# Kernel tuning notes

Hardware: AMD Instinct MI355X
Metric: run time of the kernel (lower is better)

Reference implementation:

```python
import jax, jax.numpy as jnp
import numpy as np

DIM_MODEL = 1024
DIM_K = 64
DIM_V = 64
H = 16
B = 2
S = 2048


def setup_inputs() -> dict:
    key = jax.random.key(0)
    ks = jax.random.split(key, 11)
    s = 0.02
    return {
        "Q": jax.random.normal(ks[0], (B, S, DIM_MODEL), jnp.float32),
        "K": jax.random.normal(ks[1], (B, S, DIM_MODEL), jnp.float32),
        "V": jax.random.normal(ks[2], (B, S, DIM_MODEL), jnp.float32),
        "Wq": jax.random.normal(ks[3], (DIM_MODEL, H * DIM_K), jnp.float32) * s,
        "bq": jnp.zeros((H * DIM_K,), jnp.float32),
        "Wk": jax.random.normal(ks[4], (DIM_MODEL, H * DIM_K), jnp.float32) * s,
        "bk": jnp.zeros((H * DIM_K,), jnp.float32),
        "Wv": jax.random.normal(ks[5], (DIM_MODEL, H * DIM_V), jnp.float32) * s,
        "bv": jnp.zeros((H * DIM_V,), jnp.float32),
        "Wo": jax.random.normal(ks[6], (H * DIM_V, DIM_MODEL), jnp.float32) * s,
        "bo": jnp.zeros((DIM_MODEL,), jnp.float32),
    }


def reference(Q, K, V, Wq, bq, Wk, bk, Wv, bv, Wo, bo):
    b, len_q = Q.shape[0], Q.shape[1]
    # QKV projections, split heads: [b, h, S, d]
    q = (Q @ Wq + bq).reshape(b, len_q, H, DIM_K).transpose(0, 2, 1, 3)
    k = (K @ Wk + bk).reshape(b, K.shape[1], H, DIM_K).transpose(0, 2, 1, 3)
    v = (V @ Wv + bv).reshape(b, V.shape[1], H, DIM_V).transpose(0, 2, 1, 3)
    # FAITHFUL QUIRK: original scales by sqrt(K.shape[0]) == batch size, not dim_k
    scale = 1.0 / np.sqrt(b).astype(np.float32)
    att = jnp.einsum('bhqd,bhkd->bhqk', q * scale, k)
    att = jax.nn.softmax(att, axis=-1)
    out = jnp.einsum('bhqk,bhkd->bhqd', att, v)  # [b,h,S,dv]
    out = out.transpose(0, 2, 1, 3).reshape(b, len_q, H * DIM_V)
    return out @ Wo + bo
```

## Files before the change

kernel.cpp:

```cpp
#include <hip/hip_runtime.h>
#include <hip/hip_bf16.h>


using bf16 = __hip_bfloat16;
typedef __attribute__((ext_vector_type(4))) float f32x4;
typedef __attribute__((ext_vector_type(8))) short bf16x8;

__device__ __forceinline__ void gload_lds16(const void* gsrc, void* ldst) {
    __builtin_amdgcn_global_load_lds(
        (const __attribute__((address_space(1))) void*)gsrc,
        (__attribute__((address_space(3))) void*)ldst,
        16, 0, 0);
}

__device__ __forceinline__ float fexp2(float x) {
    float r; asm("v_exp_f32 %0, %1" : "=v"(r) : "v"(x)); return r;
}

__device__ __forceinline__ unsigned cvtpk(float a, float b) {
    unsigned d; asm("v_cvt_pk_bf16_f32 %0, %1, %2" : "=v"(d) : "v"(a), "v"(b));
    return d;
}

__device__ __forceinline__ void pls32(unsigned &a, unsigned &b) {
    asm("v_permlane32_swap_b32 %0, %1" : "+v"(a), "+v"(b));
}
__device__ __forceinline__ void pls16(unsigned &a, unsigned &b) {
    asm("v_permlane16_swap_b32 %0, %1" : "+v"(a), "+v"(b));
}

__device__ __forceinline__ unsigned pack2bf(float a, float b) {
    unsigned short ua = __builtin_bit_cast(unsigned short, __float2bfloat16(a));
    unsigned short ub = __builtin_bit_cast(unsigned short, __float2bfloat16(b));
    return (unsigned)ua | ((unsigned)ub << 16);
}

__global__ void conv3_kernel(const float* __restrict__ X0, const float* __restrict__ X1,
                             const float* __restrict__ X2,
                             bf16* __restrict__ O0, bf16* __restrict__ O1, bf16* __restrict__ O2,
                             int n4) {
    int z = blockIdx.z;
    const float* in = z == 0 ? X0 : (z == 1 ? X1 : X2);
    bf16* out = z == 0 ? O0 : (z == 1 ? O1 : O2);
    int idx = blockIdx.x * blockDim.x + threadIdx.x;
    int stride = gridDim.x * blockDim.x;
    for (int i = idx; i < n4; i += stride) {
        float4 v = reinterpret_cast<const float4*>(in)[i];
        reinterpret_cast<uint2*>(out)[i] = make_uint2(pack2bf(v.x, v.y), pack2bf(v.z, v.w));
    }
}

__global__ void transpose4_kernel(const float* __restrict__ W0, const float* __restrict__ W1,
                                  const float* __restrict__ W2, const float* __restrict__ W3,
                                  bf16* __restrict__ T0, bf16* __restrict__ T1,
                                  bf16* __restrict__ T2, bf16* __restrict__ T3) {
    int z = blockIdx.z;
    const float* W = z == 0 ? W0 : (z == 1 ? W1 : (z == 2 ? W2 : W3));
    bf16* WT = z == 0 ? T0 : (z == 1 ? T1 : (z == 2 ? T2 : T3));
    __shared__ float t[32][33];
    int bx = blockIdx.x * 32, by = blockIdx.y * 32;
    int x = threadIdx.x, y = threadIdx.y;
    #pragma unroll
    for (int i = 0; i < 4; ++i)
        t[y + 8*i][x] = W[(size_t)(by + y + 8*i) * 1024 + bx + x];
    __syncthreads();
    #pragma unroll
    for (int i = 0; i < 4; ++i)
        WT[(size_t)(bx + y + 8*i) * 1024 + by + x] = __float2bfloat16(t[x][y + 8*i]);
}

template<int NTILE>
__global__ __launch_bounds__(256, 3)
void gemm_bt(const bf16* __restrict__ A0, const bf16* __restrict__ A1, const bf16* __restrict__ A2,
             const bf16* __restrict__ B0, const bf16* __restrict__ B1, const bf16* __restrict__ B2,
             const float* __restrict__ bi0, const float* __restrict__ bi1, const float* __restrict__ bi2,
             void* __restrict__ O0, void* __restrict__ O1, void* __restrict__ O2,
             int mode_base)
{
    const int f = blockIdx.x;
    int x, y, z;
    if (NTILE == 128) {
        const int s = f >> 3;
        y = s & 7;
        const int t = (f & 7) + 8 * (s >> 3);
        x = t & 31; z = t >> 5;
    } else {
        const int s = f >> 3;
        y = s & 15;
        x = (f & 7) + 8 * (s >> 4);
        z = 0;
    }
    const bf16* A  = z == 0 ? A0 : (z == 1 ? A1 : A2);
    const bf16* BT = z == 0 ? B0 : (z == 1 ? B1 : B2);
    const float* bias = z == 0 ? bi0 : (z == 1 ? bi1 : bi2);
    void* Cout = z == 0 ? O0 : (z == 1 ? O1 : O2);
    const int mode = mode_base + z;

    constexpr int MF = (NTILE == 128) ? 4 : 2;
    __shared__ __align__(16) char Abuf[16384];
    __shared__ __align__(16) char Bbuf[NTILE * 128];
    const int tid = threadIdx.x;
    const int wave = tid >> 6, lane = tid & 63;
    const int g = lane >> 4, ln = lane & 15;
    const int m0 = x * 128, n0 = y * NTILE;
    const int wm = (NTILE == 128) ? (wave >> 1) * 64 : wave * 32;
    const int wn = (NTILE == 128) ? (wave & 1) * 64 : 0;
    const int lnsw = (ln & 7) << 4;

    f32x4 acc[MF][4] = {};

    for (int k0 = 0; k0 < 1024; k0 += 64) {
        __syncthreads();
        #pragma unroll
        for (int rd = 0; rd < 4; ++rd) {
            int row = rd * 32 + (tid >> 3);
            int src = ((tid & 7) * 16) ^ (((tid >> 3) & 7) << 4);
            gload_lds16((const char*)(A + (size_t)(m0 + row) * 1024 + k0) + src,
                        Abuf + rd * 4096 + tid * 16);
        }
        #pragma unroll
        for (int rd = 0; rd < NTILE / 32; ++rd) {
            int row = rd * 32 + (tid >> 3);
            int src = ((tid & 7) * 16) ^ (((tid >> 3) & 7) << 4);
            gload_lds16((const char*)(BT + (size_t)(n0 + row) * 1024 + k0) + src,
                        Bbuf + rd * 4096 + tid * 16);
        }
        __syncthreads();
        #pragma unroll
        for (int kk = 0; kk < 2; ++kk) {
            bf16x8 af[MF], bfr[4];
            #pragma unroll
            for (int mf = 0; mf < MF; ++mf)
                af[mf] = *(const bf16x8*)&Abuf[(wm + mf*16 + ln) * 128 + ((kk*64 + g*16) ^ lnsw)];
            #pragma unroll
            for (int nf = 0; nf < 4; ++nf)
                bfr[nf] = *(const bf16x8*)&Bbuf[(wn + nf*16 + ln) * 128 + ((kk*64 + g*16) ^ lnsw)];
            #pragma unroll
            for (int mf = 0; mf < MF; ++mf)
                #pragma unroll
                for (int nf = 0; nf < 4; ++nf)
                    acc[mf][nf] = __builtin_amdgcn_mfma_f32_16x16x32_bf16(af[mf], bfr[nf], acc[mf][nf], 0, 0, 0);
        }
    }

    const float scl = (mode == 0) ? (0.70710678118654752f * 1.44269504088896340f) : 1.0f;
    #pragma unroll
    for (int mf = 0; mf < MF; ++mf) {
        #pragma unroll
        for (int nf = 0; nf < 4; ++nf) {
            int col = n0 + wn + nf*16 + ln;
            float bv = bias[col];
            #pragma unroll
            for (int r = 0; r < 4; ++r) {
                int row = m0 + wm + mf*16 + g*4 + r;
                float v = (acc[mf][nf][r] + bv) * scl;
                if (mode == 0 || mode == 1) {
                    ((bf16*)Cout)[(size_t)row * 1024 + col] = __float2bfloat16(v);
                } else if (mode == 2) {
                    int b = row >> 11, ss = row & 2047;
                    int hh = col >> 6, dv = col & 63;
                    ((bf16*)Cout)[(((size_t)(b*16 + hh) * 64 + dv) << 11) + ss] = __float2bfloat16(v);
                } else {
                    ((float*)Cout)[(size_t)row * 1024 + col] = v;
                }
            }
        }
    }
}

__global__ __launch_bounds__(256, 2)
void attn_kernel(const bf16* __restrict__ qh, const bf16* __restrict__ kh,
                 const bf16* __restrict__ vt, bf16* __restrict__ aout)
{
    __shared__ __align__(16) bf16 Kls[2][128 * 64];
    __shared__ __align__(16) bf16 Vls[2][64 * 128];
    const int f = blockIdx.x;
    const int xcd = f & 7, s = f >> 3, i = s & 15, ghi = s >> 4;
    const int bh = xcd + 8 * ghi;
    const int b = bh >> 4, h = bh & 15;
    const int q0 = i * 128;

    const int tid = threadIdx.x;
    const int wave = tid >> 6, lane = tid & 63;
    const int g = lane >> 4, ln = lane & 15;
    const int srow = lane >> 3;
    const int scol = ((lane & 7) * 16) ^ ((srow & 7) << 4);
    const int lnsw = (ln & 7) << 4;

    const bf16* kbase = kh + (size_t)(b * 2048) * 1024 + h * 64;
    const bf16* vbase = vt + (size_t)bh * 64 * 2048;

    const int vrow_in = lane >> 4;
    const int vcol16 = lane & 15;

    bf16x8 qf[2][2];
    #pragma unroll
    for (int nf = 0; nf < 2; ++nf) {
        const bf16* qrow = qh + (size_t)(b*2048 + q0 + wave*32 + nf*16 + ln) * 1024 + h*64;
        qf[nf][0] = *(const bf16x8*)(qrow + g*8);
        qf[nf][1] = *(const bf16x8*)(qrow + 32 + g*8);
    }

    auto stageKV = [&](int kv0, int buf) {
        #pragma unroll
        for (int c2 = 0; c2 < 4; ++c2) {
            int c = wave * 4 + c2;
            int krow = c * 8 + srow;
            gload_lds16((const char*)(kbase + (size_t)(kv0 + krow) * 1024) + scol,
                        (char*)&Kls[buf][0] + c * 1024);
        }
        #pragma unroll
        for (int c2 = 0; c2 < 4; ++c2) {
            int c = wave * 4 + c2;
            int vrow = c * 4 + vrow_in;
            int sc16 = vcol16 ^ (vrow & 15);
            gload_lds16((const char*)(vbase + (size_t)vrow * 2048 + kv0) + sc16 * 16,
                        (char*)&Vls[buf][0] + c * 1024);
        }
    };

    stageKV(0, 0);

    f32x4 oacc[4][2] = {};
    f32x4 lacc[2] = {};
    union PU { unsigned u[4]; bf16x8 v; };
    PU ones;
    ones.u[0] = ones.u[1] = ones.u[2] = ones.u[3] = 0x3F803F80u;

    for (int t = 0; t < 16; ++t) {
        const int cur = t & 1;
        if (t < 15) {
            stageKV((t + 1) * 128, cur ^ 1);
            asm volatile("s_waitcnt vmcnt(8)\n\ts_barrier" ::: "memory");
        } else {
            asm volatile("s_waitcnt vmcnt(0)\n\ts_barrier" ::: "memory");
        }
        __builtin_amdgcn_sched_barrier(0);

        const char* Kc = (const char*)&Kls[cur][0];
        const char* Vc = (const char*)&Vls[cur][0];

        f32x4 sacA[4][2] = {}, sacB[4][2] = {};
        __builtin_amdgcn_s_setprio(1);
        #pragma unroll
        for (int kk = 0; kk < 2; ++kk) {
            bf16x8 kf[4];
            #pragma unroll
            for (int mf = 0; mf < 4; ++mf)
                kf[mf] = *(const bf16x8*)(Kc + (mf*16 + ln) * 128 + ((kk*64 + g*16) ^ lnsw));
            #pragma unroll
            for (int mf = 0; mf < 4; ++mf)
                #pragma unroll
                for (int nf = 0; nf < 2; ++nf)
                    sacA[mf][nf] = __builtin_amdgcn_mfma_f32_16x16x32_bf16(kf[mf], qf[nf][kk], sacA[mf][nf], 0, 0, 0);
        }
        #pragma unroll
        for (int kk = 0; kk < 2; ++kk) {
            bf16x8 kf[4];
            #pragma unroll
            for (int mf = 0; mf < 4; ++mf)
                kf[mf] = *(const bf16x8*)(Kc + (64 + mf*16 + ln) * 128 + ((kk*64 + g*16) ^ lnsw));
            #pragma unroll
            for (int mf = 0; mf < 4; ++mf)
                #pragma unroll
                for (int nf = 0; nf < 2; ++nf)
                    sacB[mf][nf] = __builtin_amdgcn_mfma_f32_16x16x32_bf16(kf[mf], qf[nf][kk], sacB[mf][nf], 0, 0, 0);
        }
        __builtin_amdgcn_s_setprio(0);

        #pragma unroll
        for (int ha = 0; ha < 2; ++ha) {
            f32x4 (&sac)[4][2] = ha ? sacB : sacA;
            PU pf[2][2];
            #pragma unroll
            for (int nf = 0; nf < 2; ++nf) {
                unsigned w[4][2];
                #pragma unroll
                for (int mf = 0; mf < 4; ++mf) {
                    float e0 = fexp2(sac[mf][nf][0]);
                    float e1 = fexp2(sac[mf][nf][1]);
                    float e2 = fexp2(sac[mf][nf][2]);
                    float e3 = fexp2(sac[mf][nf][3]);
                    w[mf][0] = cvtpk(e0, e1);
                    w[mf][1] = cvtpk(e2, e3);
                }
                #pragma unroll
                for (int kk = 0; kk < 2; ++kk) {
                    #pragma unroll
                    for (int rp = 0; rp < 2; ++rp) {
                        unsigned a = w[2*kk][rp], bb = w[2*kk + 1][rp];
                        pls32(a, bb);
                        pls16(a, bb);
                        pf[nf][kk].u[rp] = a;
                        pf[nf][kk].u[2 + rp] = bb;
                    }
                }
            }
            __builtin_amdgcn_s_setprio(1);
            #pragma unroll
            for (int kk = 0; kk < 2; ++kk) {
                bf16x8 vf[4];
                #pragma unroll
                for (int mf = 0; mf < 4; ++mf)
                    vf[mf] = *(const bf16x8*)(Vc + (mf*16 + ln) * 256 + (((ha*8 + kk*4 + g) ^ ln) << 4));
                #pragma unroll
                for (int nf = 0; nf < 2; ++nf)
                    lacc[nf] = __builtin_amdgcn_mfma_f32_16x16x32_bf16(ones.v, pf[nf][kk].v, lacc[nf], 0, 0, 0);
                #pragma unroll
                for (int mf = 0; mf < 4; ++mf)
                    #pragma unroll
                    for (int nf = 0; nf < 2; ++nf)
                        oacc[mf][nf] = __builtin_amdgcn_mfma_f32_16x16x32_bf16(vf[mf], pf[nf][kk].v, oacc[mf][nf], 0, 0, 0);
            }
            __builtin_amdgcn_s_setprio(0);
        }
        __builtin_amdgcn_sched_barrier(0);
        asm volatile("s_barrier" ::: "memory");
    }

    #pragma unroll
    for (int nf = 0; nf < 2; ++nf) {
        float inv = 1.0f / lacc[nf][0];
        int q = q0 + wave*32 + nf*16 + ln;
        bf16* orow = aout + (size_t)(b*2048 + q) * 1024 + h * 64;
        #pragma unroll
        for (int mf = 0; mf < 4; ++mf) {
            *(uint2*)(orow + mf*16 + g*4) = make_uint2(
                pack2bf(oacc[mf][nf][0] * inv, oacc[mf][nf][1] * inv),
                pack2bf(oacc[mf][nf][2] * inv, oacc[mf][nf][3] * inv));
        }
    }
}

extern "C" void kernel_launch(void* const* d_in, const int* in_sizes, int n_in,
                              void* d_out, int out_size, void* d_ws, size_t ws_size,
                              hipStream_t stream)
{
    const float* Q  = (const float*)d_in[0];
    const float* K  = (const float*)d_in[1];
    const float* V  = (const float*)d_in[2];
    const float* Wq = (const float*)d_in[3];
    const float* bq = (const float*)d_in[4];
    const float* Wk = (const float*)d_in[5];
    const float* bk = (const float*)d_in[6];
    const float* Wv = (const float*)d_in[7];
    const float* bv = (const float*)d_in[8];
    const float* Wo = (const float*)d_in[9];
    const float* bo = (const float*)d_in[10];

    char* ws = (char*)d_ws;
    const size_t MB = 1024 * 1024;
    bf16* Qbf  = (bf16*)(ws + 0);
    bf16* Kbf  = (bf16*)(ws + 8*MB);
    bf16* Vbf  = (bf16*)(ws + 16*MB);
    bf16* WqT  = (bf16*)(ws + 24*MB);
    bf16* WkT  = (bf16*)(ws + 26*MB);
    bf16* WvT  = (bf16*)(ws + 28*MB);
    bf16* WoT  = (bf16*)(ws + 30*MB);
    bf16* qhp  = (bf16*)(ws + 32*MB);
    bf16* khp  = (bf16*)(ws + 40*MB);
    bf16* vtp  = (bf16*)(ws + 48*MB);
    bf16* aout = (bf16*)(ws + 0);

    const int n4 = (2 * 2048 * 1024) / 4;
    conv3_kernel<<<dim3(512, 1, 3), 256, 0, stream>>>(Q, K, V, Qbf, Kbf, Vbf, n4);

    transpose4_kernel<<<dim3(32, 32, 4), dim3(32, 8), 0, stream>>>(Wq, Wk, Wv, Wo, WqT, WkT, WvT, WoT);

    gemm_bt<128><<<768, 256, 0, stream>>>(Qbf, Kbf, Vbf, WqT, WkT, WvT,
                                          bq, bk, bv, qhp, khp, vtp, 0);

    attn_kernel<<<512, 256, 0, stream>>>(qhp, khp, vtp, aout);

    gemm_bt<64><<<512, 256, 0, stream>>>(aout, aout, aout, WoT, WoT, WoT,
                                         bo, bo, bo, d_out, d_out, d_out, 3);
}
```

Before: 115.4 us.

## Fuse fp32-to-bf16 input conversion into QKV GEMM and restructure attention wave split

Drops the separate fp32-to-bf16 conversion kernel. The QKV projection GEMM now loads fp32 activations straight into LDS and converts them to bf16 while building fragments, which removes a full write and re-read of Q, K and V at the cost of twice the A-tile LDS traffic. The attention kernel is also reorganised: each wave now handles 64 queries against half of each KV tile instead of 32 queries against the full tile. Row sums are computed with scalar adds and shuffles rather than a ones-MFMA, and the two KV-half partial outputs are combined through LDS at the end, which adds register pressure and an extra LDS reduction.

New measurement: 114.9 us. About the same (-0.4%).

```diff
diff --git a/kernel.cpp b/kernel.cpp
--- a/kernel.cpp
+++ b/kernel.cpp
@@ -33,21 +33,6 @@
     unsigned short ua = __builtin_bit_cast(unsigned short, __float2bfloat16(a));
     unsigned short ub = __builtin_bit_cast(unsigned short, __float2bfloat16(b));
     return (unsigned)ua | ((unsigned)ub << 16);
-}
-
-__global__ void conv3_kernel(const float* __restrict__ X0, const float* __restrict__ X1,
-                             const float* __restrict__ X2,
-                             bf16* __restrict__ O0, bf16* __restrict__ O1, bf16* __restrict__ O2,
-                             int n4) {
-    int z = blockIdx.z;
-    const float* in = z == 0 ? X0 : (z == 1 ? X1 : X2);
-    bf16* out = z == 0 ? O0 : (z == 1 ? O1 : O2);
-    int idx = blockIdx.x * blockDim.x + threadIdx.x;
-    int stride = gridDim.x * blockDim.x;
-    for (int i = idx; i < n4; i += stride) {
-        float4 v = reinterpret_cast<const float4*>(in)[i];
-        reinterpret_cast<uint2*>(out)[i] = make_uint2(pack2bf(v.x, v.y), pack2bf(v.z, v.w));
-    }
 }
 
 __global__ void transpose4_kernel(const float* __restrict__ W0, const float* __restrict__ W1,
@@ -69,9 +54,9 @@
         WT[(size_t)(bx + y + 8*i) * 1024 + by + x] = __float2bfloat16(t[x][y + 8*i]);
 }
 
-template<int NTILE>
+template<int NTILE, bool AF32>
 __global__ __launch_bounds__(256, 3)
-void gemm_bt(const bf16* __restrict__ A0, const bf16* __restrict__ A1, const bf16* __restrict__ A2,
+void gemm_bt(const void* __restrict__ A0, const void* __restrict__ A1, const void* __restrict__ A2,
              const bf16* __restrict__ B0, const bf16* __restrict__ B1, const bf16* __restrict__ B2,
              const float* __restrict__ bi0, const float* __restrict__ bi1, const float* __restrict__ bi2,
              void* __restrict__ O0, void* __restrict__ O1, void* __restrict__ O2,
@@ -90,14 +75,14 @@
         x = (f & 7) + 8 * (s >> 4);
         z = 0;
     }
-    const bf16* A  = z == 0 ? A0 : (z == 1 ? A1 : A2);
+    const void* Av = z == 0 ? A0 : (z == 1 ? A1 : A2);
     const bf16* BT = z == 0 ? B0 : (z == 1 ? B1 : B2);
     const float* bias = z == 0 ? bi0 : (z == 1 ? bi1 : bi2);
     void* Cout = z == 0 ? O0 : (z == 1 ? O1 : O2);
     const int mode = mode_base + z;
 
     constexpr int MF = (NTILE == 128) ? 4 : 2;
-    __shared__ __align__(16) char Abuf[16384];
+    __shared__ __align__(16) char Abuf[AF32 ? 32768 : 16384];
     __shared__ __align__(16) char Bbuf[NTILE * 128];
     const int tid = threadIdx.x;
     const int wave = tid >> 6, lane = tid & 63;
@@ -112,29 +97,54 @@
     for (int k0 = 0; k0 < 1024; k0 += 64) {
         __syncthreads();
         #pragma unroll
-        for (int rd = 0; rd < 4; ++rd) {
-            int row = rd * 32 + (tid >> 3);
-            int src = ((tid & 7) * 16) ^ (((tid >> 3) & 7) << 4);
-            gload_lds16((const char*)(A + (size_t)(m0 + row) * 1024 + k0) + src,
-                        Abuf + rd * 4096 + tid * 16);
-        }
-        #pragma unroll
         for (int rd = 0; rd < NTILE / 32; ++rd) {
             int row = rd * 32 + (tid >> 3);
             int src = ((tid & 7) * 16) ^ (((tid >> 3) & 7) << 4);
             gload_lds16((const char*)(BT + (size_t)(n0 + row) * 1024 + k0) + src,
                         Bbuf + rd * 4096 + tid * 16);
         }
+        if (AF32) {
+            #pragma unroll
+            for (int rd = 0; rd < 8; ++rd) {
+                int row = rd * 16 + (tid >> 4);
+                int src = ((tid & 15) * 16) ^ ((row & 15) << 4);
+                gload_lds16((const char*)((const float*)Av + (size_t)(m0 + row) * 1024 + k0) + src,
+                            Abuf + rd * 4096 + tid * 16);
+            }
+        } else {
+            #pragma unroll
+            for (int rd = 0; rd < 4; ++rd) {
+                int row = rd * 32 + (tid >> 3);
+                int src = ((tid & 7) * 16) ^ (((tid >> 3) & 7) << 4);
+                gload_lds16((const char*)((const bf16*)Av + (size_t)(m0 + row) * 1024 + k0) + src,
+                            Abuf + rd * 4096 + tid * 16);
+            }
+        }
         __syncthreads();
         #pragma unroll
         for (int kk = 0; kk < 2; ++kk) {
             bf16x8 af[MF], bfr[4];
             #pragma unroll
-            for (int mf = 0; mf < MF; ++mf)
-                af[mf] = *(const bf16x8*)&Abuf[(wm + mf*16 + ln) * 128 + ((kk*64 + g*16) ^ lnsw)];
-            #pragma unroll
-            for (int nf = 0; nf < 4; ++nf)
-                bfr[nf] = *(const bf16x8*)&Bbuf[(wn + nf*16 + ln) * 128 + ((kk*64 + g*16) ^ lnsw)];
+            for (int mf = 0; mf < MF; ++mf) {
+                int row = wm + mf * 16 + ln;
+                if (AF32) {
+                    int c0 = kk * 128 + g * 32;
+                    int sw = (row & 15) << 4;
+                    f32x4 v0 = *(const f32x4*)(Abuf + row * 256 + (c0 ^ sw));
+                    f32x4 v1 = *(const f32x4*)(Abuf + row * 256 + ((c0 + 16) ^ sw));
+                    union { unsigned u[4]; bf16x8 v; } afu;
+                    afu.u[0] = cvtpk(v0[0], v0[1]); afu.u[1] = cvtpk(v0[2], v0[3]);
+                    afu.u[2] = cvtpk(v1[0], v1[1]); afu.u[3] = cvtpk(v1[2], v1[3]);
+                    af[mf] = afu.v;
+                } else {
+                    af[mf] = *(const bf16x8*)&Abuf[row * 128 + ((kk*64 + g*16) ^ ((row & 7) << 4))];
+                }
+            }
+            #pragma unroll
+            for (int nf = 0; nf < 4; ++nf) {
+                int row = wn + nf * 16 + ln;
+                bfr[nf] = *(const bf16x8*)&Bbuf[row * 128 + ((kk*64 + g*16) ^ ((row & 7) << 4))];
+            }
             #pragma unroll
             for (int mf = 0; mf < MF; ++mf)
                 #pragma unroll
@@ -169,7 +179,7 @@
 }
 
 __global__ __launch_bounds__(256, 2)
-void attn_kernel(const bf16* __restrict__ qh, const bf16* __restrict__ kh,
+void attn_kernel(const bf16* __restrict__ qh_, const bf16* __restrict__ kh,
                  const bf16* __restrict__ vt, bf16* __restrict__ aout)
 {
     __shared__ __align__(16) bf16 Kls[2][128 * 64];
@@ -182,21 +192,22 @@
 
     const int tid = threadIdx.x;
     const int wave = tid >> 6, lane = tid & 63;
+    const int qh = wave >> 1, kvh = wave & 1;
     const int g = lane >> 4, ln = lane & 15;
     const int srow = lane >> 3;
     const int scol = ((lane & 7) * 16) ^ ((srow & 7) << 4);
     const int lnsw = (ln & 7) << 4;
+    const int vrow_in = lane >> 4, vcol16 = lane & 15;
 
     const bf16* kbase = kh + (size_t)(b * 2048) * 1024 + h * 64;
     const bf16* vbase = vt + (size_t)bh * 64 * 2048;
-
-    const int vrow_in = lane >> 4;
-    const int vcol16 = lane & 15;
-
-    bf16x8 qf[2][2];
-    #pragma unroll
-    for (int nf = 0; nf < 2; ++nf) {
-        const bf16* qrow = qh + (size_t)(b*2048 + q0 + wave*32 + nf*16 + ln) * 1024 + h*64;
+    char* Kb = (char*)&Kls[0][0];
+    char* Vb = (char*)&Vls[0][0];
+
+    bf16x8 qf[4][2];
+    #pragma unroll
+    for (int nf = 0; nf < 4; ++nf) {
+        const bf16* qrow = qh_ + (size_t)(b*2048 + q0 + qh*64 + nf*16 + ln) * 1024 + h*64;
         qf[nf][0] = *(const bf16x8*)(qrow + g*8);
         qf[nf][1] = *(const bf16x8*)(qrow + 32 + g*8);
     }
@@ -207,7 +218,7 @@
             int c = wave * 4 + c2;
             int krow = c * 8 + srow;
             gload_lds16((const char*)(kbase + (size_t)(kv0 + krow) * 1024) + scol,
-                        (char*)&Kls[buf][0] + c * 1024);
+                        Kb + buf * 16384 + c * 1024);
         }
         #pragma unroll
         for (int c2 = 0; c2 < 4; ++c2) {
@@ -215,17 +226,15 @@
             int vrow = c * 4 + vrow_in;
             int sc16 = vcol16 ^ (vrow & 15);
             gload_lds16((const char*)(vbase + (size_t)vrow * 2048 + kv0) + sc16 * 16,
-                        (char*)&Vls[buf][0] + c * 1024);
+                        Vb + buf * 16384 + c * 1024);
         }
     };
 
     stageKV(0, 0);
 
-    f32x4 oacc[4][2] = {};
-    f32x4 lacc[2] = {};
+    f32x4 oacc[4][4] = {};
+    float lsum[4] = {0.f, 0.f, 0.f, 0.f};
     union PU { unsigned u[4]; bf16x8 v; };
-    PU ones;
-    ones.u[0] = ones.u[1] = ones.u[2] = ones.u[3] = 0x3F803F80u;
 
     for (int t = 0; t < 16; ++t) {
         const int cur = t & 1;
@@ -237,97 +246,110 @@
         }
         __builtin_amdgcn_sched_barrier(0);
 
-        const char* Kc = (const char*)&Kls[cur][0];
-        const char* Vc = (const char*)&Vls[cur][0];
-
-        f32x4 sacA[4][2] = {}, sacB[4][2] = {};
+        const char* Kc = Kb + cur * 16384;
+        const char* Vc = Vb + cur * 16384;
+
+        f32x4 sac[4][4] = {};
         __builtin_amdgcn_s_setprio(1);
         #pragma unroll
         for (int kk = 0; kk < 2; ++kk) {
             bf16x8 kf[4];
             #pragma unroll
-            for (int mf = 0; mf < 4; ++mf)
-                kf[mf] = *(const bf16x8*)(Kc + (mf*16 + ln) * 128 + ((kk*64 + g*16) ^ lnsw));
+            for (int mf = 0; mf < 4; ++mf) {
+                int row = kvh*64 + mf*16 + ln;
+                kf[mf] = *(const bf16x8*)(Kc + row * 128 + ((kk*64 + g*16) ^ lnsw));
+            }
             #pragma unroll
             for (int mf = 0; mf < 4; ++mf)
                 #pragma unroll
-                for (int nf = 0; nf < 2; ++nf)
-                    sacA[mf][nf] = __builtin_amdgcn_mfma_f32_16x16x32_bf16(kf[mf], qf[nf][kk], sacA[mf][nf], 0, 0, 0);
-        }
+                for (int nf = 0; nf < 4; ++nf)
+                    sac[mf][nf] = __builtin_amdgcn_mfma_f32_16x16x32_bf16(kf[mf], qf[nf][kk], sac[mf][nf], 0, 0, 0);
+        }
+        __builtin_amdgcn_s_setprio(0);
+        __builtin_amdgcn_sched_barrier(0);
+
+        PU pf[4][2];
+        #pragma unroll
+        for (int nf = 0; nf < 4; ++nf) {
+            unsigned w[4][2];
+            #pragma unroll
+            for (int mf = 0; mf < 4; ++mf) {
+                float e0 = fexp2(sac[mf][nf][0]);
+                float e1 = fexp2(sac[mf][nf][1]);
+                float e2 = fexp2(sac[mf][nf][2]);
+                float e3 = fexp2(sac[mf][nf][3]);
+                lsum[nf] += (e0 + e1) + (e2 + e3);
+                w[mf][0] = cvtpk(e0, e1);
+                w[mf][1] = cvtpk(e2, e3);
+            }
+            #pragma unroll
+            for (int kk = 0; kk < 2; ++kk) {
+                #pragma unroll
+                for (int rp = 0; rp < 2; ++rp) {
+                    unsigned a = w[2*kk][rp], bb = w[2*kk + 1][rp];
+                    pls32(a, bb);
+                    pls16(a, bb);
+                    pf[nf][kk].u[rp] = a;
+                    pf[nf][kk].u[2 + rp] = bb;
+                }
+            }
+        }
+
+        __builtin_amdgcn_s_setprio(1);
         #pragma unroll
         for (int kk = 0; kk < 2; ++kk) {
-            bf16x8 kf[4];
-            #pragma unroll
-            for (int mf = 0; mf < 4; ++mf)
-                kf[mf] = *(const bf16x8*)(Kc + (64 + mf*16 + ln) * 128 + ((kk*64 + g*16) ^ lnsw));
+            bf16x8 vf[4];
+            #pragma unroll
+            for (int mf = 0; mf < 4; ++mf) {
+                int row = mf*16 + ln;
+                vf[mf] = *(const bf16x8*)(Vc + row * 256 + (((kvh*8 + kk*4 + g) ^ ln) << 4));
+            }
             #pragma unroll
             for (int mf = 0; mf < 4; ++mf)
                 #pragma unroll
-                for (int nf = 0; nf < 2; ++nf)
-                    sacB[mf][nf] = __builtin_amdgcn_mfma_f32_16x16x32_bf16(kf[mf], qf[nf][kk], sacB[mf][nf], 0, 0, 0);
+                for (int nf = 0; nf < 4; ++nf)
+                    oacc[mf][nf] = __builtin_amdgcn_mfma_f32_16x16x32_bf16(vf[mf], pf[nf][kk].v, oacc[mf][nf], 0, 0, 0);
         }
         __builtin_amdgcn_s_setprio(0);
-
-        #pragma unroll
-        for (int ha = 0; ha < 2; ++ha) {
-            f32x4 (&sac)[4][2] = ha ? sacB : sacA;
-            PU pf[2][2];
-            #pragma unroll
-            for (int nf = 0; nf < 2; ++nf) {
-                unsigned w[4][2];
-                #pragma unroll
-                for (int mf = 0; mf < 4; ++mf) {
-                    float e0 = fexp2(sac[mf][nf][0]);
-                    float e1 = fexp2(sac[mf][nf][1]);
-                    float e2 = fexp2(sac[mf][nf][2]);
-                    float e3 = fexp2(sac[mf][nf][3]);
-                    w[mf][0] = cvtpk(e0, e1);
-                    w[mf][1] = cvtpk(e2, e3);
-                }
-                #pragma unroll
-                for (int kk = 0; kk < 2; ++kk) {
-                    #pragma unroll
-                    for (int rp = 0; rp < 2; ++rp) {
-                        unsigned a = w[2*kk][rp], bb = w[2*kk + 1][rp];
-                        pls32(a, bb);
-                        pls16(a, bb);
-                        pf[nf][kk].u[rp] = a;
-                        pf[nf][kk].u[2 + rp] = bb;
-                    }
-                }
-            }
-            __builtin_amdgcn_s_setprio(1);
-            #pragma unroll
-            for (int kk = 0; kk < 2; ++kk) {
-                bf16x8 vf[4];
-                #pragma unroll
-                for (int mf = 0; mf < 4; ++mf)
-                    vf[mf] = *(const bf16x8*)(Vc + (mf*16 + ln) * 256 + (((ha*8 + kk*4 + g) ^ ln) << 4));
-                #pragma unroll
-                for (int nf = 0; nf < 2; ++nf)
-                    lacc[nf] = __builtin_amdgcn_mfma_f32_16x16x32_bf16(ones.v, pf[nf][kk].v, lacc[nf], 0, 0, 0);
-                #pragma unroll
-                for (int mf = 0; mf < 4; ++mf)
-                    #pragma unroll
-                    for (int nf = 0; nf < 2; ++nf)
-                        oacc[mf][nf] = __builtin_amdgcn_mfma_f32_16x16x32_bf16(vf[mf], pf[nf][kk].v, oacc[mf][nf], 0, 0, 0);
-            }
-            __builtin_amdgcn_s_setprio(0);
-        }
         __builtin_amdgcn_sched_barrier(0);
-        asm volatile("s_barrier" ::: "memory");
-    }
-
-    #pragma unroll
-    for (int nf = 0; nf < 2; ++nf) {
-        float inv = 1.0f / lacc[nf][0];
-        int q = q0 + wave*32 + nf*16 + ln;
-        bf16* orow = aout + (size_t)(b*2048 + q) * 1024 + h * 64;
-        #pragma unroll
-        for (int mf = 0; mf < 4; ++mf) {
-            *(uint2*)(orow + mf*16 + g*4) = make_uint2(
-                pack2bf(oacc[mf][nf][0] * inv, oacc[mf][nf][1] * inv),
-                pack2bf(oacc[mf][nf][2] * inv, oacc[mf][nf][3] * inv));
+        asm volatile("s_waitcnt lgkmcnt(0)\n\ts_barrier" ::: "memory");
+    }
+
+    #pragma unroll
+    for (int nf = 0; nf < 4; ++nf) {
+        float l = lsum[nf];
+        l += __shfl_xor(l, 16);
+        l += __shfl_xor(l, 32);
+        lsum[nf] = l;
+    }
+    __syncthreads();
+    float* Lb = (float*)Vb;
+    if (kvh == 1) {
+        #pragma unroll
+        for (int mf = 0; mf < 4; ++mf)
+            #pragma unroll
+            for (int nf = 0; nf < 4; ++nf)
+                *(f32x4*)(Kb + qh * 16384 + (mf*4 + nf) * 1024 + lane * 16) = oacc[mf][nf];
+        #pragma unroll
+        for (int nf = 0; nf < 4; ++nf)
+            Lb[qh * 256 + nf * 64 + lane] = lsum[nf];
+    }
+    __syncthreads();
+    if (kvh == 0) {
+        #pragma unroll
+        for (int nf = 0; nf < 4; ++nf) {
+            float inv = 1.0f / (lsum[nf] + Lb[qh * 256 + nf * 64 + lane]);
+            int q = q0 + qh*64 + nf*16 + ln;
+            bf16* orow = aout + (size_t)(b*2048 + q) * 1024 + h * 64;
+            #pragma unroll
+            for (int mf = 0; mf < 4; ++mf) {
+                f32x4 o2 = *(const f32x4*)(Kb + qh * 16384 + (mf*4 + nf) * 1024 + lane * 16);
+                float v0 = (oacc[mf][nf][0] + o2[0]) * inv;
+                float v1 = (oacc[mf][nf][1] + o2[1]) * inv;
+                float v2 = (oacc[mf][nf][2] + o2[2]) * inv;
+                float v3 = (oacc[mf][nf][3] + o2[3]) * inv;
+                *(uint2*)(orow + mf*16 + g*4) = make_uint2(pack2bf(v0, v1), pack2bf(v2, v3));
+            }
         }
     }
 }
@@ -350,9 +372,6 @@
 
     char* ws = (char*)d_ws;
     const size_t MB = 1024 * 1024;
-    bf16* Qbf  = (bf16*)(ws + 0);
-    bf16* Kbf  = (bf16*)(ws + 8*MB);
-    bf16* Vbf  = (bf16*)(ws + 16*MB);
     bf16* WqT  = (bf16*)(ws + 24*MB);
     bf16* WkT  = (bf16*)(ws + 26*MB);
     bf16* WvT  = (bf16*)(ws + 28*MB);
@@ -362,16 +381,13 @@
     bf16* vtp  = (bf16*)(ws + 48*MB);
     bf16* aout = (bf16*)(ws + 0);
 
-    const int n4 = (2 * 2048 * 1024) / 4;
-    conv3_kernel<<<dim3(512, 1, 3), 256, 0, stream>>>(Q, K, V, Qbf, Kbf, Vbf, n4);
-
     transpose4_kernel<<<dim3(32, 32, 4), dim3(32, 8), 0, stream>>>(Wq, Wk, Wv, Wo, WqT, WkT, WvT, WoT);
 
-    gemm_bt<128><<<768, 256, 0, stream>>>(Qbf, Kbf, Vbf, WqT, WkT, WvT,
-                                          bq, bk, bv, qhp, khp, vtp, 0);
+    gemm_bt<128, true><<<768, 256, 0, stream>>>(Q, K, V, WqT, WkT, WvT,
+                                                bq, bk, bv, qhp, khp, vtp, 0);
 
     attn_kernel<<<512, 256, 0, stream>>>(qhp, khp, vtp, aout);
 
-    gemm_bt<64><<<512, 256, 0, stream>>>(aout, aout, aout, WoT, WoT, WoT,
-                                         bo, bo, bo, d_out, d_out, d_out, 3);
-}
+    gemm_bt<64, false><<<512, 256, 0, stream>>>(aout, aout, aout, WoT, WoT, WoT,
+                                                bo, bo, bo, d_out, d_out, d_out, 3);
+}
```
